# Optimization experiments

Hardware: AMD Instinct MI355X
Metric: run time of the kernel (lower is better)

## Reference

```python
import jax, jax.numpy as jnp
import numpy as np
import math

MARGIN = 0.2
INVALID = -0.1


def fourier_embedding(positions, dimension):
    # positions: [B, C, 2] in [0, 1]; returns [B, C, dimension]
    n_freqs = int(math.isqrt(dimension // 2))  # 32 for dim=2048
    width = 1.0 + 2.0 * MARGIN
    freqs = jnp.arange(n_freqs, dtype=positions.dtype)
    p_x = (2.0 * math.pi / width) * freqs[:, None]  # [n, 1]
    p_y = (2.0 * math.pi / width) * freqs           # [n]
    pos = positions + MARGIN                        # [B, C, 2]
    # loc[b,c,i,j] = pos_x * p_x[i] + pos_y * p_y[j]
    loc = pos[..., 0, None, None] * p_x + pos[..., 1, None, None] * p_y
    loc = loc.reshape(*positions.shape[:-1], n_freqs * n_freqs)  # [B, C, n^2]
    return jnp.concatenate([jnp.cos(loc), jnp.sin(loc)], axis=-1)


def setup_inputs() -> dict:
    key = jax.random.key(0)
    k1, k2, k3 = jax.random.split(key, 3)
    B, C, T = 64, 270, 2000
    O, D = 270, 2048  # merger_channels, embedding_dim
    x = jax.random.normal(k1, (B, C, T), dtype=jnp.float32)
    layout = jax.random.uniform(k2, (C, 2), dtype=jnp.float32)
    heads = jax.random.normal(k3, (O, D), dtype=jnp.float32) / (D ** 0.5)
    return {"x": x, "layout": layout, "heads": heads}


def reference(x, layout, heads):
    # x: [B, C, T]; layout: [C, 2]; heads: [O, D]
    B, C, T = x.shape
    O, D = heads.shape
    # PositionGetter: broadcast layout to all batch items (len(layout) == C here,
    # so no INVALID padding rows exist, but we keep the mask math for fidelity).
    positions = jnp.broadcast_to(layout[None], (B, C, 2))
    invalid = jnp.all(positions == INVALID, axis=-1)          # [B, C]
    score_offset = jnp.where(invalid, -jnp.inf, 0.0).astype(x.dtype)
    embedding = fourier_embedding(positions, D)               # [B, C, D]
    scores = jnp.einsum('bcd,od->boc', embedding, heads)      # [B, O, C]
    scores = scores + score_offset[:, None, :]
    weights = jax.nn.softmax(scores, axis=2)                  # [B, O, C]
    out = jnp.einsum('bct,boc->bot', x, weights)              # [B, O, T]
    return out
```

## Files before the change

### kernel.cpp

```cpp
#include <hip/hip_runtime.h>
#include <math.h>

typedef float f32x4 __attribute__((ext_vector_type(4)));
typedef short bf16x8 __attribute__((ext_vector_type(8)));

#define SCALE 4.48798950512827605495f

#define SCORES_OFF 0
#define WH_OFF     311040
#define WL_OFF     476928
#define EMBH_OFF   642816
#define HEADSH_OFF 1748736

__device__ __forceinline__ unsigned short bf16rn(float f) {
    unsigned int u = __float_as_uint(f);
    u += 0x7FFFu + ((u >> 16) & 1u);
    return (unsigned short)(u >> 16);
}

__global__ void prep_kernel(const float* __restrict__ layout,
                            const float* __restrict__ heads,
                            unsigned short* __restrict__ embh,
                            unsigned short* __restrict__ headsh) {
    int blk = blockIdx.x;
    if (blk < 270) {
        int c = blk;
        float px = (layout[2 * c] + 0.2f) * SCALE;
        float py = (layout[2 * c + 1] + 0.2f) * SCALE;
        unsigned short* row = embh + (size_t)c * 2048;
        for (int q = threadIdx.x; q < 1024; q += blockDim.x) {
            int i = q >> 5, j = q & 31;
            float loc = px * (float)i + py * (float)j;
            float s, co;
            sincosf(loc, &s, &co);
            row[q] = bf16rn(co);
            row[1024 + q] = bf16rn(s);
        }
    } else {
        int o = blk - 270;
        const float* src = heads + (size_t)o * 2048;
        unsigned short* dst = headsh + (size_t)o * 2048;
        for (int q = threadIdx.x; q < 2048; q += blockDim.x)
            dst[q] = bf16rn(src[q]);
    }
}

__global__ __launch_bounds__(64) void scores_kernel(
    const unsigned short* __restrict__ headsh,
    const unsigned short* __restrict__ embh,
    float* __restrict__ scores)
{
    const int ot = blockIdx.x, ct = blockIdx.y, kc = blockIdx.z;
    const int lane = threadIdx.x;
    const int lhi = lane >> 4, llo = lane & 15;
    f32x4 acc[2][2];
    #pragma unroll
    for (int m = 0; m < 2; ++m)
        #pragma unroll
        for (int n = 0; n < 2; ++n) acc[m][n] = (f32x4){0.f, 0.f, 0.f, 0.f};

    const int k0 = kc * 256;
    #pragma unroll
    for (int ks = 0; ks < 8; ++ks) {
        int kk = k0 + ks * 32 + lhi * 8;
        bf16x8 a[2], bb[2];
        #pragma unroll
        for (int m = 0; m < 2; ++m) {
            int row = ot * 32 + m * 16 + llo; if (row > 269) row = 269;
            a[m] = *(const bf16x8*)(headsh + (size_t)row * 2048 + kk);
        }
        #pragma unroll
        for (int n = 0; n < 2; ++n) {
            int crow = ct * 32 + n * 16 + llo; if (crow > 269) crow = 269;
            bb[n] = *(const bf16x8*)(embh + (size_t)crow * 2048 + kk);
        }
        #pragma unroll
        for (int m = 0; m < 2; ++m)
            #pragma unroll
            for (int n = 0; n < 2; ++n)
                acc[m][n] = __builtin_amdgcn_mfma_f32_16x16x32_bf16(a[m], bb[n], acc[m][n], 0, 0, 0);
    }
    #pragma unroll
    for (int m = 0; m < 2; ++m)
        #pragma unroll
        for (int n = 0; n < 2; ++n)
            #pragma unroll
            for (int r = 0; r < 4; ++r) {
                int row = ot * 32 + m * 16 + lhi * 4 + r;
                int col = ct * 32 + n * 16 + llo;
                if (row < 270 && col < 270)
                    atomicAdd(&scores[row * 288 + col], acc[m][n][r]);
            }
}

__global__ void softmax_kernel(const float* __restrict__ scores,
                               const float* __restrict__ layout,
                               unsigned short* __restrict__ Wh,
                               unsigned short* __restrict__ Wl) {
    int o = blockIdx.x;
    int lane = threadIdx.x;
    unsigned short* wh = Wh + (size_t)o * 288;
    unsigned short* wl = Wl + (size_t)o * 288;
    if (o >= 270) {
        for (int c = lane; c < 288; c += 64) { wh[c] = 0; wl[c] = 0; }
        return;
    }
    float v[5]; int cs[5]; int n = 0;
    float m = -INFINITY;
    for (int c = lane; c < 270; c += 64) {
        float s = scores[o * 288 + c];
        bool inv = (layout[c * 2] == -0.1f) && (layout[c * 2 + 1] == -0.1f);
        if (inv) s = -INFINITY;
        v[n] = s; cs[n] = c; n++;
        m = fmaxf(m, s);
    }
    for (int off = 32; off >= 1; off >>= 1) m = fmaxf(m, __shfl_xor(m, off));
    float sum = 0.f;
    for (int k = 0; k < n; ++k) { v[k] = expf(v[k] - m); sum += v[k]; }
    for (int off = 32; off >= 1; off >>= 1) sum += __shfl_xor(sum, off);
    float inv_s = 1.f / sum;
    for (int k = 0; k < n; ++k) {
        float w = v[k] * inv_s;
        unsigned int wb = __float_as_uint(w);
        unsigned short hi = (unsigned short)(wb >> 16);
        float whf = __uint_as_float(wb & 0xFFFF0000u);
        wh[cs[k]] = hi;
        wl[cs[k]] = (unsigned short)(__float_as_uint(w - whf) >> 16);
    }
    for (int c = 270 + lane; c < 288; c += 64) { wh[c] = 0; wl[c] = 0; }
}

__global__ __launch_bounds__(256, 2) void merge_kernel(
    const float* __restrict__ x,
    const unsigned short* __restrict__ Wh,
    const unsigned short* __restrict__ Wl,
    float* __restrict__ out)
{
    __shared__ float xs[2][32][128];
    const int tb = blockIdx.x, ob = blockIdx.y, b = blockIdx.z;
    const int t0 = tb * 128, o0 = ob * 96;
    const int tid = threadIdx.x;
    const int wid = tid >> 6, lane = tid & 63;
    const int wo = (wid >> 1) * 48, wt = (wid & 1) * 64;
    const int lhi = lane >> 4, llo = lane & 15;

    const float* xb = x + (size_t)b * 270 * 2000;
    const float* x_last = x + (size_t)64 * 270 * 2000 - 4;

    f32x4 acc[3][4];
    #pragma unroll
    for (int m = 0; m < 3; ++m)
        #pragma unroll
        for (int n = 0; n < 4; ++n) acc[m][n] = (f32x4){0.f, 0.f, 0.f, 0.f};

    int s_row[4], s_col4[4];
    #pragma unroll
    for (int i = 0; i < 4; ++i) {
        int f = tid + (i << 8);
        s_row[i] = f >> 5;
        s_col4[i] = f & 31;
    }
    f32x4 stg[4];

    auto load_tile = [&](int ks) {
        #pragma unroll
        for (int i = 0; i < 4; ++i) {
            int c = ks * 32 + s_row[i];
            if (c > 269) c = 269;
            const float* p = xb + (size_t)c * 2000 + t0 + (s_col4[i] << 2);
            if (p > x_last) p = x_last;
            stg[i] = *(const f32x4*)p;
        }
    };
    auto store_tile = [&](int buf) {
        #pragma unroll
        for (int i = 0; i < 4; ++i) {
            int cs = s_col4[i] ^ ((s_row[i] >> 2) & 7);
            *(f32x4*)&xs[buf][s_row[i]][cs << 2] = stg[i];
        }
    };

    load_tile(0);
    store_tile(0);
    __syncthreads();

    for (int ks = 0; ks < 9; ++ks) {
        const int cur = ks & 1;
        if (ks < 8) load_tile(ks + 1);

        bf16x8 ah[3], al[3];
        #pragma unroll
        for (int m = 0; m < 3; ++m) {
            int row = o0 + wo + m * 16 + llo;
            size_t off = (size_t)row * 288 + ks * 32 + lhi * 8;
            ah[m] = *(const bf16x8*)(Wh + off);
            al[m] = *(const bf16x8*)(Wl + off);
        }

        #pragma unroll
        for (int nf = 0; nf < 4; ++nf) {
            int tcol = wt + nf * 16 + llo;
            float xr[8];
            #pragma unroll
            for (int j = 0; j < 8; ++j) {
                int k = lhi * 8 + j;
                int cidx = tcol ^ (((k >> 2) & 7) << 2);
                xr[j] = xs[cur][k][cidx];
            }
            union { unsigned int u[4]; bf16x8 v; } bh, bl;
            #pragma unroll
            for (int p = 0; p < 4; ++p) {
                unsigned int u0 = __float_as_uint(xr[2 * p]);
                unsigned int u1 = __float_as_uint(xr[2 * p + 1]);
                bh.u[p] = (u0 >> 16) | (u1 & 0xFFFF0000u);
                float h0 = __uint_as_float(u0 & 0xFFFF0000u);
                float h1 = __uint_as_float(u1 & 0xFFFF0000u);
                unsigned int l0 = __float_as_uint(xr[2 * p] - h0);
                unsigned int l1 = __float_as_uint(xr[2 * p + 1] - h1);
                bl.u[p] = (l0 >> 16) | (l1 & 0xFFFF0000u);
            }
            #pragma unroll
            for (int m = 0; m < 3; ++m) {
                acc[m][nf] = __builtin_amdgcn_mfma_f32_16x16x32_bf16(ah[m], bh.v, acc[m][nf], 0, 0, 0);
                acc[m][nf] = __builtin_amdgcn_mfma_f32_16x16x32_bf16(ah[m], bl.v, acc[m][nf], 0, 0, 0);
                acc[m][nf] = __builtin_amdgcn_mfma_f32_16x16x32_bf16(al[m], bh.v, acc[m][nf], 0, 0, 0);
            }
        }

        if (ks < 8) store_tile(cur ^ 1);
        __syncthreads();
    }

    const size_t ob_base = (size_t)b * 270 * 2000;
    #pragma unroll
    for (int m = 0; m < 3; ++m) {
        #pragma unroll
        for (int r = 0; r < 4; ++r) {
            int orow = o0 + wo + m * 16 + lhi * 4 + r;
            if (orow < 270) {
                float* op = out + ob_base + (size_t)orow * 2000;
                #pragma unroll
                for (int nf = 0; nf < 4; ++nf) {
                    int t = t0 + wt + nf * 16 + llo;
                    if (t < 2000) op[t] = acc[m][nf][r];
                }
            }
        }
    }
}

extern "C" void kernel_launch(void* const* d_in, const int* in_sizes, int n_in,
                              void* d_out, int out_size, void* d_ws, size_t ws_size,
                              hipStream_t stream) {
    const float* x      = (const float*)d_in[0];
    const float* layout = (const float*)d_in[1];
    const float* heads  = (const float*)d_in[2];
    float* out = (float*)d_out;
    char* ws = (char*)d_ws;

    float* scores          = (float*)(ws + SCORES_OFF);
    unsigned short* Wh     = (unsigned short*)(ws + WH_OFF);
    unsigned short* Wl     = (unsigned short*)(ws + WL_OFF);
    unsigned short* embh   = (unsigned short*)(ws + EMBH_OFF);
    unsigned short* headsh = (unsigned short*)(ws + HEADSH_OFF);

    hipMemsetAsync(scores, 0, 270 * 288 * 4, stream);
    prep_kernel<<<540, 256, 0, stream>>>(layout, heads, embh, headsh);
    scores_kernel<<<dim3(9, 9, 8), 64, 0, stream>>>(headsh, embh, scores);
    softmax_kernel<<<288, 64, 0, stream>>>(scores, layout, Wh, Wl);
    merge_kernel<<<dim3(16, 3, 64), 256, 0, stream>>>(x, Wh, Wl, out);
}
```

Baseline: 330.5 us.

## Replace split-K atomics with in-block reduction and widen merge tiles

The scores GEMM now splits K across four waves of one block and reduces the partials in shared memory, which removes the global atomicAdds and the memset. The merge kernel doubles its time tile to 256 columns, and each wave now covers all 96 output rows over 64 time columns, so x tiles are reused across more outputs and W fragments are loaded once per wave for 6 row-groups. In exchange the merge kernel holds twice the accumulator registers (24 f32x4) and twice the shared memory, which may lower occupancy under launch_bounds(256,2). Its grid also halves to 8x3x64 blocks.

```diff
diff --git a/kernel.cpp b/kernel.cpp
--- a/kernel.cpp
+++ b/kernel.cpp
@@ -45,52 +45,70 @@
     }
 }
 
-__global__ __launch_bounds__(64) void scores_kernel(
+__global__ __launch_bounds__(256) void scores_kernel(
     const unsigned short* __restrict__ headsh,
     const unsigned short* __restrict__ embh,
     float* __restrict__ scores)
 {
-    const int ot = blockIdx.x, ct = blockIdx.y, kc = blockIdx.z;
-    const int lane = threadIdx.x;
+    __shared__ float red[4][64][16];
+    const int ot = blockIdx.x, ct = blockIdx.y;
+    const int tid = threadIdx.x;
+    const int w = tid >> 6, lane = tid & 63;
     const int lhi = lane >> 4, llo = lane & 15;
+
     f32x4 acc[2][2];
     #pragma unroll
     for (int m = 0; m < 2; ++m)
         #pragma unroll
         for (int n = 0; n < 2; ++n) acc[m][n] = (f32x4){0.f, 0.f, 0.f, 0.f};
 
-    const int k0 = kc * 256;
-    #pragma unroll
-    for (int ks = 0; ks < 8; ++ks) {
-        int kk = k0 + ks * 32 + lhi * 8;
+    int arow[2], crow[2];
+    #pragma unroll
+    for (int m = 0; m < 2; ++m) {
+        int r = ot * 32 + m * 16 + llo; arow[m] = (r > 269) ? 269 : r;
+        int c = ct * 32 + m * 16 + llo; crow[m] = (c > 269) ? 269 : c;
+    }
+
+    for (int s = 0; s < 16; ++s) {
+        int kk = w * 512 + s * 32 + lhi * 8;
         bf16x8 a[2], bb[2];
         #pragma unroll
-        for (int m = 0; m < 2; ++m) {
-            int row = ot * 32 + m * 16 + llo; if (row > 269) row = 269;
-            a[m] = *(const bf16x8*)(headsh + (size_t)row * 2048 + kk);
-        }
-        #pragma unroll
-        for (int n = 0; n < 2; ++n) {
-            int crow = ct * 32 + n * 16 + llo; if (crow > 269) crow = 269;
-            bb[n] = *(const bf16x8*)(embh + (size_t)crow * 2048 + kk);
-        }
+        for (int m = 0; m < 2; ++m)
+            a[m] = *(const bf16x8*)(headsh + (size_t)arow[m] * 2048 + kk);
+        #pragma unroll
+        for (int n = 0; n < 2; ++n)
+            bb[n] = *(const bf16x8*)(embh + (size_t)crow[n] * 2048 + kk);
         #pragma unroll
         for (int m = 0; m < 2; ++m)
             #pragma unroll
             for (int n = 0; n < 2; ++n)
                 acc[m][n] = __builtin_amdgcn_mfma_f32_16x16x32_bf16(a[m], bb[n], acc[m][n], 0, 0, 0);
     }
+
     #pragma unroll
     for (int m = 0; m < 2; ++m)
         #pragma unroll
         for (int n = 0; n < 2; ++n)
             #pragma unroll
-            for (int r = 0; r < 4; ++r) {
-                int row = ot * 32 + m * 16 + lhi * 4 + r;
-                int col = ct * 32 + n * 16 + llo;
-                if (row < 270 && col < 270)
-                    atomicAdd(&scores[row * 288 + col], acc[m][n][r]);
-            }
+            for (int r = 0; r < 4; ++r)
+                red[w][lane][m * 8 + n * 4 + r] = acc[m][n][r];
+    __syncthreads();
+    if (w == 0) {
+        #pragma unroll
+        for (int m = 0; m < 2; ++m)
+            #pragma unroll
+            for (int n = 0; n < 2; ++n)
+                #pragma unroll
+                for (int r = 0; r < 4; ++r) {
+                    int idx = m * 8 + n * 4 + r;
+                    float sum = red[0][lane][idx] + red[1][lane][idx]
+                              + red[2][lane][idx] + red[3][lane][idx];
+                    int row = ot * 32 + m * 16 + lhi * 4 + r;
+                    int col = ct * 32 + n * 16 + llo;
+                    if (row < 270 && col < 270)
+                        scores[row * 288 + col] = sum;
+                }
+    }
 }
 
 __global__ void softmax_kernel(const float* __restrict__ scores,
@@ -136,47 +154,40 @@
     const unsigned short* __restrict__ Wl,
     float* __restrict__ out)
 {
-    __shared__ float xs[2][32][128];
+    __shared__ float xs[2][32][256];
     const int tb = blockIdx.x, ob = blockIdx.y, b = blockIdx.z;
-    const int t0 = tb * 128, o0 = ob * 96;
+    const int t0 = tb * 256, o0 = ob * 96;
     const int tid = threadIdx.x;
     const int wid = tid >> 6, lane = tid & 63;
-    const int wo = (wid >> 1) * 48, wt = (wid & 1) * 64;
+    const int wt = wid * 64;
     const int lhi = lane >> 4, llo = lane & 15;
 
     const float* xb = x + (size_t)b * 270 * 2000;
     const float* x_last = x + (size_t)64 * 270 * 2000 - 4;
 
-    f32x4 acc[3][4];
-    #pragma unroll
-    for (int m = 0; m < 3; ++m)
+    f32x4 acc[6][4];
+    #pragma unroll
+    for (int m = 0; m < 6; ++m)
         #pragma unroll
         for (int n = 0; n < 4; ++n) acc[m][n] = (f32x4){0.f, 0.f, 0.f, 0.f};
 
-    int s_row[4], s_col4[4];
-    #pragma unroll
-    for (int i = 0; i < 4; ++i) {
-        int f = tid + (i << 8);
-        s_row[i] = f >> 5;
-        s_col4[i] = f & 31;
-    }
-    f32x4 stg[4];
-
+    f32x4 stg[8];
     auto load_tile = [&](int ks) {
         #pragma unroll
-        for (int i = 0; i < 4; ++i) {
-            int c = ks * 32 + s_row[i];
+        for (int p = 0; p < 8; ++p) {
+            int c = ks * 32 + p * 4 + wid;
             if (c > 269) c = 269;
-            const float* p = xb + (size_t)c * 2000 + t0 + (s_col4[i] << 2);
-            if (p > x_last) p = x_last;
-            stg[i] = *(const f32x4*)p;
+            const float* ptr = xb + (size_t)c * 2000 + t0 + (lane << 2);
+            if (ptr > x_last) ptr = x_last;
+            stg[p] = *(const f32x4*)ptr;
         }
     };
     auto store_tile = [&](int buf) {
         #pragma unroll
-        for (int i = 0; i < 4; ++i) {
-            int cs = s_col4[i] ^ ((s_row[i] >> 2) & 7);
-            *(f32x4*)&xs[buf][s_row[i]][cs << 2] = stg[i];
+        for (int p = 0; p < 8; ++p) {
+            int row = p * 4 + wid;
+            int cs = lane ^ ((row >> 2) & 7);
+            *(f32x4*)&xs[buf][row][cs << 2] = stg[p];
         }
     };
 
@@ -188,10 +199,10 @@
         const int cur = ks & 1;
         if (ks < 8) load_tile(ks + 1);
 
-        bf16x8 ah[3], al[3];
-        #pragma unroll
-        for (int m = 0; m < 3; ++m) {
-            int row = o0 + wo + m * 16 + llo;
+        bf16x8 ah[6], al[6];
+        #pragma unroll
+        for (int m = 0; m < 6; ++m) {
+            int row = o0 + m * 16 + llo;
             size_t off = (size_t)row * 288 + ks * 32 + lhi * 8;
             ah[m] = *(const bf16x8*)(Wh + off);
             al[m] = *(const bf16x8*)(Wl + off);
@@ -220,7 +231,7 @@
                 bl.u[p] = (l0 >> 16) | (l1 & 0xFFFF0000u);
             }
             #pragma unroll
-            for (int m = 0; m < 3; ++m) {
+            for (int m = 0; m < 6; ++m) {
                 acc[m][nf] = __builtin_amdgcn_mfma_f32_16x16x32_bf16(ah[m], bh.v, acc[m][nf], 0, 0, 0);
                 acc[m][nf] = __builtin_amdgcn_mfma_f32_16x16x32_bf16(ah[m], bl.v, acc[m][nf], 0, 0, 0);
                 acc[m][nf] = __builtin_amdgcn_mfma_f32_16x16x32_bf16(al[m], bh.v, acc[m][nf], 0, 0, 0);
@@ -233,10 +244,10 @@
 
     const size_t ob_base = (size_t)b * 270 * 2000;
     #pragma unroll
-    for (int m = 0; m < 3; ++m) {
+    for (int m = 0; m < 6; ++m) {
         #pragma unroll
         for (int r = 0; r < 4; ++r) {
-            int orow = o0 + wo + m * 16 + lhi * 4 + r;
+            int orow = o0 + m * 16 + lhi * 4 + r;
             if (orow < 270) {
                 float* op = out + ob_base + (size_t)orow * 2000;
                 #pragma unroll
@@ -264,9 +275,8 @@
     unsigned short* embh   = (unsigned short*)(ws + EMBH_OFF);
     unsigned short* headsh = (unsigned short*)(ws + HEADSH_OFF);
 
-    hipMemsetAsync(scores, 0, 270 * 288 * 4, stream);
     prep_kernel<<<540, 256, 0, stream>>>(layout, heads, embh, headsh);
-    scores_kernel<<<dim3(9, 9, 8), 64, 0, stream>>>(headsh, embh, scores);
+    scores_kernel<<<dim3(9, 9), 256, 0, stream>>>(headsh, embh, scores);
     softmax_kernel<<<288, 64, 0, stream>>>(scores, layout, Wh, Wl);
-    merge_kernel<<<dim3(16, 3, 64), 256, 0, stream>>>(x, Wh, Wl, out);
-}
+    merge_kernel<<<dim3(8, 3, 64), 256, 0, stream>>>(x, Wh, Wl, out);
+}
```

After: 315.9 us. 4.4% less time.
